# Performance work log

Hardware: AMD Instinct MI355X
Metric: run time of the kernel (lower is better)

## Reference

```python
import jax, jax.numpy as jnp
import numpy as np

jax.config.update("jax_enable_x64", True)

BATCH = 64
NUM_TRAJ = 128
MAXT = 1.0
DELTAT = 2.0 ** -8
N_STEPS = int(round(MAXT / DELTAT)) - 1  # tvec = arange(0, maxt, dt): 256 points -> 255 Euler steps

_sx = np.array([[0, 1], [1, 0]], dtype=np.complex128)
_sy = np.array([[0, -1j], [1j, 0]], dtype=np.complex128)
_sz = np.array([[1, 0], [0, -1]], dtype=np.complex128)
_I2 = np.eye(2, dtype=np.complex128)

# Two-qubit Rabi weak-measurement operators (d=10 Hermitian state, m=2 noise channels)
HX = jnp.asarray(0.5 * (np.kron(_sx, _I2) + np.kron(_I2, _sx)))  # Rabi drive
HZ = jnp.asarray(0.5 * (np.kron(_sz, _I2) + np.kron(_I2, _sz)))  # detuning
C1 = jnp.asarray(np.kron(_sz, _I2))  # weak measurement channel, qubit 0
C2 = jnp.asarray(np.kron(_I2, _sz))  # weak measurement channel, qubit 1


def _meas_ops():
    # 42 probabilities: 9 joint Pauli-basis pairs x 4 outcomes (36) + single-qubit '+' outcomes (6)
    paulis = [_sx, _sy, _sz]
    ops = []
    for A in paulis:
        for B in paulis:
            for sa in (1, -1):
                for sb in (1, -1):
                    ops.append(np.kron((_I2 + sa * A) / 2, (_I2 + sb * B) / 2))
    for A in paulis:
        ops.append(np.kron((_I2 + A) / 2, _I2))
    for B in paulis:
        ops.append(np.kron(_I2, (_I2 + B) / 2))
    return jnp.asarray(np.stack(ops))  # [42, 4, 4]

MEAS = _meas_ops()


def _forward(inputs, params, wvec, rho0):
    inputs = inputs.astype(jnp.float64)  # [B, 1]
    batch = inputs.shape[0]

    # Build per-trajectory params: column input_param=0 comes from inputs, rest are constants
    cols = [inputs + 1e-8 if ii == 0 else params[ii].astype(jnp.float64) * jnp.ones_like(inputs)
            for ii in range(params.shape[0])]
    traj_p = jnp.concatenate(cols, axis=1)            # [B, 4]
    traj_p = jnp.tile(traj_p, (NUM_TRAJ, 1))          # [N, 4], N = NUM_TRAJ*B
    N = NUM_TRAJ * batch

    rho = jnp.tile(rho0[None].astype(jnp.complex128), (N, 1, 1))  # [N, 4, 4]

    Omega = traj_p[:, 0].astype(jnp.complex128)[:, None, None]
    eps = traj_p[:, 1].astype(jnp.complex128)[:, None, None]
    Gamma = traj_p[:, 2][:, None, None]               # real
    eta = traj_p[:, 3][:, None, None]                 # real, measurement efficiency
    H = Omega * HX + eps * HZ                         # [N, 4, 4]
    sqge = jnp.sqrt(jnp.maximum(Gamma * eta, 0.0))

    def hmeas(r, c):
        # H[c] rho = c rho + rho c - tr(c rho + rho c) rho  (c Hermitian)
        anti = c @ r + r @ c
        tr = jnp.trace(anti, axis1=-2, axis2=-1)[:, None, None]
        return anti - tr * r

    def step(r, dw):                                  # dw: [N, 2] real, ~sqrt(dt) Gaussian
        comm = H @ r - r @ H
        diss = (C1 @ r @ C1 - r) + (C2 @ r @ C2 - r)  # c^2 = I for sigma_z channels
        drift = -1j * comm + Gamma * diss
        noise = sqge * (hmeas(r, C1) * dw[:, 0, None, None]
                        + hmeas(r, C2) * dw[:, 1, None, None])
        return r + drift * DELTAT + noise, None

    dws = jnp.swapaxes(wvec.astype(jnp.float64), 0, 1)  # [T-1, N, 2]
    rho_T, _ = jax.lax.scan(step, rho, dws)

    # Monte-Carlo average over num_traj (matches reduce_mean over axis 0 of [num_traj, B, ...])
    rho_mean = jnp.mean(rho_T.reshape(NUM_TRAJ, batch, 4, 4), axis=0)  # [B, 4, 4]

    probs = jnp.real(jnp.einsum('kij,bji->bk', MEAS, rho_mean))        # tr(M rho), [B, 42]
    probs = jnp.clip(probs, 0.0, 1.0)
    out = jnp.concatenate([probs, inputs], axis=1)                     # [B, 43]
    return out, rho_mean


def setup_inputs() -> dict:
    key = jax.random.key(0)
    k1, k2 = jax.random.split(key)
    inputs = jax.random.uniform(k1, (BATCH, 1), dtype=jnp.float64)
    params = jnp.array([1.0, 0.1, 0.5, 0.8], dtype=jnp.float64)  # [Omega, eps, Gamma, eta]
    wvec = jax.random.normal(k2, (NUM_TRAJ * BATCH, N_STEPS, 2), dtype=jnp.float64) * np.sqrt(DELTAT)
    rho0 = jnp.zeros((4, 4), dtype=jnp.complex128).at[0, 0].set(1.0)  # |00><00|
    return {"inputs": inputs, "params": params, "wvec": wvec, "rho0": rho0}


def reference(inputs, params, wvec, rho0):
    return _forward(inputs, params, wvec, rho0)
```

## Files before the change

### kernel.cpp

```cpp
#include <hip/hip_runtime.h>
#include <math.h>

#define BATCH 64
#define NUM_TRAJ 128
#define NTOT (BATCH*NUM_TRAJ)
#define NSTEPS 255

static constexpr float DT = 0.00390625f;

template<int C>
__device__ __forceinline__ float qp(float x) {
    union { float f; int i; } u;
    u.f = x;
    u.i = __builtin_amdgcn_update_dpp(0, u.i, C, 0xF, 0xF, true);
    return u.f;
}
#define DPP_HALF_MIRROR 0x141

__device__ __forceinline__ float qsum2(float x) { return qp<65>(x) + qp<190>(x); }

__global__ __launch_bounds__(64) void traj_kernel(
    const float* __restrict__ inputs,
    const float* __restrict__ params,
    const float* __restrict__ wvec,
    const float* __restrict__ rho0,
    int rho0_cplx,
    float* __restrict__ ws)
{
    const int tid = blockIdx.x * 64 + threadIdx.x;
    const int g  = tid >> 3;
    const int l8 = tid & 7;
    const int p  = l8 & 3;
    const int c  = l8 >> 2;
    const int r  = c ? (3 - p) : p;
    const int b  = g & (BATCH - 1);

    const float Omega = inputs[b] + 1e-8f;
    const float a     = 0.5f * Omega;
    const float eps   = params[1];
    const float Gamma = params[2];
    const float eta   = params[3];
    const float sqge  = sqrtf(fmaxf(Gamma * eta, 0.0f));
    const float gdt   = Gamma * DT;

    const float s1   = (r < 2) ? 1.0f : -1.0f;
    const float s2   = (r & 1) ? -1.0f : 1.0f;
    const float hr   = (r == 0) ? eps : ((r == 3) ? -eps : 0.0f);
    const int  colA  = c ? 1 : 0;
    const int  colB  = c ? 2 : 3;
    const float s2A  = c ? -1.0f : 1.0f;
    const float coefA = hr - (c ? 0.0f : eps);
    const float coefB = hr + (c ? 0.0f : eps);
    const float dmA  = gdt * ( (s1 + s2 * s2A) - 2.0f);
    const float dmB  = gdt * (-(s1 + s2 * s2A) - 2.0f);
    const float S1   = s1 * sqge;
    const float S2   = s2 * sqge;
    const float SQ   = sqge;
    const float PC2  = (c ? -1.0f : 1.0f) * sqge;
    const float f1   = (r == colA) ? 1.0f : 0.0f;
    const float f2   = (r == colB) ? 1.0f : 0.0f;

    float qa_re, qa_im, qb_re, qb_im;
    {
        const int idxA = r * 4 + colA, idxB = r * 4 + colB;
        if (rho0_cplx) {
            qa_re = rho0[2 * idxA]; qa_im = rho0[2 * idxA + 1];
            qb_re = rho0[2 * idxB]; qb_im = rho0[2 * idxB + 1];
        } else {
            qa_re = rho0[idxA]; qa_im = 0.0f;
            qb_re = rho0[idxB]; qb_im = 0.0f;
        }
    }

    const float2* wp2 = reinterpret_cast<const float2*>(wvec) + (size_t)g * NSTEPS;

    auto step = [&](float dwA, float dwB) {
        const float u_re = qa_re + qb_re, u_im = qa_im + qb_im;
        const float up_re = qp<DPP_HALF_MIRROR>(u_re);
        const float up_im = qp<DPP_HALF_MIRROR>(u_im);

        const float pown = fmaf(S1, dwA, S2 * dwB);
        const float tw = pown + pown;
        const float tm_re = tw * fmaf(f1, qa_re, f2 * qb_re);
        const float tm_im = tw * fmaf(f1, qa_im, f2 * qb_im);

        const float SA_re = qsum2(qa_re), SA_im = qsum2(qa_im);
        const float SB_re = qsum2(qb_re), SB_im = qsum2(qb_im);

        const float cA_re = fmaf(coefA, qa_re, a * (SA_re - up_re));
        const float cA_im = fmaf(coefA, qa_im, a * (SA_im - up_im));
        const float cB_re = fmaf(coefB, qb_re, a * (SB_re - up_re));
        const float cB_im = fmaf(coefB, qb_im, a * (SB_im - up_im));

        float z_re = tm_re, z_im = tm_im;
        z_re += qp<177>(z_re); z_im += qp<177>(z_im);
        z_re += qp<78>(z_re);  z_im += qp<78>(z_im);
        z_re += qp<DPP_HALF_MIRROR>(z_re);
        z_im += qp<DPP_HALF_MIRROR>(z_im);
        const float ur = z_re, ui = z_im;

        const float pc   = fmaf(SQ, dwA, PC2 * dwB);
        const float base = pown - ur;
        const float WA = (base + dmA) + pc;
        const float WB = (base + dmB) - pc;

        float n_re, n_im;
        n_re = fmaf(DT, cA_im, qa_re);  n_re = fmaf(WA, qa_re, n_re); n_re = fmaf( ui, qa_im, n_re);
        n_im = fmaf(-DT, cA_re, qa_im); n_im = fmaf(WA, qa_im, n_im); n_im = fmaf(-ui, qa_re, n_im);
        qa_re = n_re; qa_im = n_im;
        n_re = fmaf(DT, cB_im, qb_re);  n_re = fmaf(WB, qb_re, n_re); n_re = fmaf( ui, qb_im, n_re);
        n_im = fmaf(-DT, cB_re, qb_im); n_im = fmaf(WB, qb_im, n_im); n_im = fmaf(-ui, qb_re, n_im);
        qb_re = n_re; qb_im = n_im;
    };

    float2 cw[8], nw[8];
#pragma unroll
    for (int s = 0; s < 8; ++s) cw[s] = wp2[s];
#pragma unroll 1
    for (int T = 0; T < 31; ++T) {
        if (T < 30) {
#pragma unroll
            for (int s = 0; s < 8; ++s) nw[s] = wp2[8 * (T + 1) + s];
        } else {
#pragma unroll
            for (int s = 0; s < 7; ++s) nw[s] = wp2[248 + s];
            nw[7] = make_float2(0.f, 0.f);
        }
#pragma unroll
        for (int s = 0; s < 8; ++s) step(cw[s].x, cw[s].y);
#pragma unroll
        for (int s = 0; s < 8; ++s) cw[s] = nw[s];
    }
#pragma unroll
    for (int s = 0; s < 7; ++s) step(cw[s].x, cw[s].y);

    float4* o = reinterpret_cast<float4*>(ws + (size_t)g * 32);
    o[c * 4 + r] = make_float4(qa_re, qa_im, qb_re, qb_im);
}

__device__ inline void fill_proj(int p, float s, float pr[2][2], float pim[2][2])
{
    pr[0][0] = 0.5f; pr[0][1] = 0.f; pr[1][0] = 0.f; pr[1][1] = 0.5f;
    pim[0][0] = 0.f; pim[0][1] = 0.f; pim[1][0] = 0.f; pim[1][1] = 0.f;
    const float h = 0.5f * s;
    if (p == 0)      { pr[0][1] += h;  pr[1][0] += h; }
    else if (p == 1) { pim[0][1] -= h; pim[1][0] += h; }
    else             { pr[0][0] += h;  pr[1][1] -= h; }
}

__device__ inline void fill_id(float pr[2][2], float pim[2][2])
{
    pr[0][0] = 1.f; pr[0][1] = 0.f; pr[1][0] = 0.f; pr[1][1] = 1.f;
    pim[0][0] = 0.f; pim[0][1] = 0.f; pim[1][0] = 0.f; pim[1][1] = 0.f;
}

__global__ __launch_bounds__(256) void reduce_meas_kernel(
    const float* __restrict__ ws,
    const float* __restrict__ inputs,
    float* __restrict__ out,
    int out_size)
{
    const int b = blockIdx.x;
    const int tid = threadIdx.x;
    __shared__ float part[8][32];
    __shared__ float sr[16], si[16];

    {
        const int e = tid & 31;
        const int h = tid >> 5;
        const int plane = e >> 4;
        const int el = e & 15;
        const int i = el >> 2, j = el & 3;
        const int cc = (j == 1 || j == 2) ? 1 : 0;
        const int slot = (j == 2 || j == 3) ? 1 : 0;
        const int fidx = (cc * 4 + i) * 4 + slot * 2 + plane;
        float s = 0.f;
#pragma unroll 4
        for (int k = h * 16; k < h * 16 + 16; k++)
            s += ws[((size_t)(k * BATCH + b)) * 32 + fidx];
        part[h][e] = s;
    }
    __syncthreads();
    if (tid < 32) {
        float s = 0.f;
#pragma unroll
        for (int h = 0; h < 8; h++) s += part[h][tid];
        s *= (1.0f / NUM_TRAJ);
        if (tid < 16) sr[tid] = s; else si[tid - 16] = s;
    }
    __syncthreads();

    if (tid < 42) {
        float par[2][2], pai[2][2], pbr[2][2], pbi[2][2];
        const int m = tid;
        if (m < 36) {
            const int ia = m / 12, rem = m - ia * 12;
            const int ib = rem / 4, r2 = rem - ib * 4;
            fill_proj(ia, (r2 & 2) ? -1.f : 1.f, par, pai);
            fill_proj(ib, (r2 & 1) ? -1.f : 1.f, pbr, pbi);
        } else if (m < 39) {
            fill_proj(m - 36, 1.f, par, pai);
            fill_id(pbr, pbi);
        } else {
            fill_id(par, pai);
            fill_proj(m - 39, 1.f, pbr, pbi);
        }
        float prob = 0.f;
#pragma unroll
        for (int a1 = 0; a1 < 2; a1++)
#pragma unroll
            for (int b1 = 0; b1 < 2; b1++)
#pragma unroll
                for (int a2 = 0; a2 < 2; a2++)
#pragma unroll
                    for (int b2 = 0; b2 < 2; b2++) {
                        const int i = 2 * a1 + b1, j = 2 * a2 + b2;
                        const float Mr = par[a1][a2] * pbr[b1][b2] - pai[a1][a2] * pbi[b1][b2];
                        const float Mi = par[a1][a2] * pbi[b1][b2] + pai[a1][a2] * pbr[b1][b2];
                        prob += Mr * sr[j * 4 + i] - Mi * si[j * 4 + i];
                    }
        prob = fminf(fmaxf(prob, 0.f), 1.f);
        out[b * 43 + m] = prob;
    } else if (tid == 42) {
        out[b * 43 + 42] = inputs[b];
    }

    if (out_size >= 2752 + 2048) {
        if (tid < 16) {
            out[2752 + b * 32 + 2 * tid]     = sr[tid];
            out[2752 + b * 32 + 2 * tid + 1] = si[tid];
        }
    } else if (out_size >= 2752 + 1024) {
        if (tid < 16) out[2752 + b * 16 + tid] = sr[tid];
    }
}

extern "C" void kernel_launch(void* const* d_in, const int* in_sizes, int n_in,
                              void* d_out, int out_size, void* d_ws, size_t ws_size,
                              hipStream_t stream)
{
    const float* inputs = (const float*)d_in[0];
    const float* params = (const float*)d_in[1];
    const float* wvec   = (const float*)d_in[2];
    const float* rho0   = (const float*)d_in[3];
    const int rho0_cplx = (n_in > 3 && in_sizes[3] >= 32) ? 1 : 0;
    float* ws = (float*)d_ws;

    traj_kernel<<<(NTOT * 8) / 64, 64, 0, stream>>>(inputs, params, wvec, rho0, rho0_cplx, ws);
    reduce_meas_kernel<<<BATCH, 256, 0, stream>>>(ws, inputs, (float*)d_out, out_size);
}
```

Before: 36.01 us.

## Split each trajectory across 16 lanes, one density-matrix element per lane

Each trajectory's 4x4 density matrix is now spread over 16 lanes, one complex element each, where before it was 8 lanes holding two elements each. Cross-lane sums use an added row-rotate-by-8 DPP step, and the workspace layout plus the reduce kernel's indexing are updated to match. The aim is to shorten the serial dependency chain per Euler step and double the number of wavefronts, so latency is hidden better across 255 sequential steps. In exchange, twice as many threads each load the same noise values, and every step needs extra DPP operations.

```diff
diff --git a/kernel.cpp b/kernel.cpp
--- a/kernel.cpp
+++ b/kernel.cpp
@@ -16,6 +16,7 @@
     return u.f;
 }
 #define DPP_HALF_MIRROR 0x141
+#define DPP_ROR8        0x128
 
 __device__ __forceinline__ float qsum2(float x) { return qp<65>(x) + qp<190>(x); }
 
@@ -28,12 +29,15 @@
     float* __restrict__ ws)
 {
     const int tid = blockIdx.x * 64 + threadIdx.x;
-    const int g  = tid >> 3;
-    const int l8 = tid & 7;
-    const int p  = l8 & 3;
-    const int c  = l8 >> 2;
-    const int r  = c ? (3 - p) : p;
-    const int b  = g & (BATCH - 1);
+    const int g   = tid >> 4;
+    const int L   = tid & 15;
+    const int hh  = L >> 3;
+    const int l8  = L & 7;
+    const int p   = l8 & 3;
+    const int c   = l8 >> 2;
+    const int r   = c ? (3 - p) : p;
+    const int col = hh ? (c ? 2 : 3) : (c ? 1 : 0);
+    const int b   = g & (BATCH - 1);
 
     const float Omega = inputs[b] + 1e-8f;
     const float a     = 0.5f * Omega;
@@ -43,74 +47,62 @@
     const float sqge  = sqrtf(fmaxf(Gamma * eta, 0.0f));
     const float gdt   = Gamma * DT;
 
-    const float s1   = (r < 2) ? 1.0f : -1.0f;
-    const float s2   = (r & 1) ? -1.0f : 1.0f;
-    const float hr   = (r == 0) ? eps : ((r == 3) ? -eps : 0.0f);
-    const int  colA  = c ? 1 : 0;
-    const int  colB  = c ? 2 : 3;
-    const float s2A  = c ? -1.0f : 1.0f;
-    const float coefA = hr - (c ? 0.0f : eps);
-    const float coefB = hr + (c ? 0.0f : eps);
-    const float dmA  = gdt * ( (s1 + s2 * s2A) - 2.0f);
-    const float dmB  = gdt * (-(s1 + s2 * s2A) - 2.0f);
-    const float S1   = s1 * sqge;
-    const float S2   = s2 * sqge;
-    const float SQ   = sqge;
-    const float PC2  = (c ? -1.0f : 1.0f) * sqge;
-    const float f1   = (r == colA) ? 1.0f : 0.0f;
-    const float f2   = (r == colB) ? 1.0f : 0.0f;
-
-    float qa_re, qa_im, qb_re, qb_im;
+    const float s1r = (r   < 2) ? 1.0f : -1.0f;
+    const float s2r = (r   & 1) ? -1.0f : 1.0f;
+    const float s1c = (col < 2) ? 1.0f : -1.0f;
+    const float s2c = (col & 1) ? -1.0f : 1.0f;
+    const float hr  = (r   == 0) ? eps : ((r   == 3) ? -eps : 0.0f);
+    const float hc  = (col == 0) ? eps : ((col == 3) ? -eps : 0.0f);
+    const float coef = hr - hc;
+    const float dm  = gdt * (s1r * s1c + s2r * s2c - 2.0f);
+    const float S1  = s1r * sqge;
+    const float S2  = s2r * sqge;
+    const float PA  = s1c * sqge;
+    const float PB  = s2c * sqge;
+    const float f   = (r == col) ? 1.0f : 0.0f;
+    const float FA  = 2.0f * f * S1;
+    const float FB  = 2.0f * f * S2;
+
+    float x_re, x_im;
     {
-        const int idxA = r * 4 + colA, idxB = r * 4 + colB;
-        if (rho0_cplx) {
-            qa_re = rho0[2 * idxA]; qa_im = rho0[2 * idxA + 1];
-            qb_re = rho0[2 * idxB]; qb_im = rho0[2 * idxB + 1];
-        } else {
-            qa_re = rho0[idxA]; qa_im = 0.0f;
-            qb_re = rho0[idxB]; qb_im = 0.0f;
-        }
+        const int idx = r * 4 + col;
+        if (rho0_cplx) { x_re = rho0[2 * idx]; x_im = rho0[2 * idx + 1]; }
+        else           { x_re = rho0[idx];     x_im = 0.0f; }
     }
 
     const float2* wp2 = reinterpret_cast<const float2*>(wvec) + (size_t)g * NSTEPS;
 
     auto step = [&](float dwA, float dwB) {
-        const float u_re = qa_re + qb_re, u_im = qa_im + qb_im;
+        const float u_re = x_re + qp<DPP_ROR8>(x_re);
+        const float u_im = x_im + qp<DPP_ROR8>(x_im);
         const float up_re = qp<DPP_HALF_MIRROR>(u_re);
         const float up_im = qp<DPP_HALF_MIRROR>(u_im);
 
+        const float S_re = qsum2(x_re);
+        const float S_im = qsum2(x_im);
+
+        const float cm_re = fmaf(coef, x_re, a * (S_re - up_re));
+        const float cm_im = fmaf(coef, x_im, a * (S_im - up_im));
+
+        const float t = fmaf(FA, dwA, FB * dwB);
+        float z_re = t * x_re, z_im = t * x_im;
+        z_re += qp<177>(z_re);             z_im += qp<177>(z_im);
+        z_re += qp<78>(z_re);              z_im += qp<78>(z_im);
+        z_re += qp<DPP_HALF_MIRROR>(z_re); z_im += qp<DPP_HALF_MIRROR>(z_im);
+        z_re += qp<DPP_ROR8>(z_re);        z_im += qp<DPP_ROR8>(z_im);
+        const float ur = z_re, ui = z_im;
+
         const float pown = fmaf(S1, dwA, S2 * dwB);
-        const float tw = pown + pown;
-        const float tm_re = tw * fmaf(f1, qa_re, f2 * qb_re);
-        const float tm_im = tw * fmaf(f1, qa_im, f2 * qb_im);
-
-        const float SA_re = qsum2(qa_re), SA_im = qsum2(qa_im);
-        const float SB_re = qsum2(qb_re), SB_im = qsum2(qb_im);
-
-        const float cA_re = fmaf(coefA, qa_re, a * (SA_re - up_re));
-        const float cA_im = fmaf(coefA, qa_im, a * (SA_im - up_im));
-        const float cB_re = fmaf(coefB, qb_re, a * (SB_re - up_re));
-        const float cB_im = fmaf(coefB, qb_im, a * (SB_im - up_im));
-
-        float z_re = tm_re, z_im = tm_im;
-        z_re += qp<177>(z_re); z_im += qp<177>(z_im);
-        z_re += qp<78>(z_re);  z_im += qp<78>(z_im);
-        z_re += qp<DPP_HALF_MIRROR>(z_re);
-        z_im += qp<DPP_HALF_MIRROR>(z_im);
-        const float ur = z_re, ui = z_im;
-
-        const float pc   = fmaf(SQ, dwA, PC2 * dwB);
-        const float base = pown - ur;
-        const float WA = (base + dmA) + pc;
-        const float WB = (base + dmB) - pc;
-
-        float n_re, n_im;
-        n_re = fmaf(DT, cA_im, qa_re);  n_re = fmaf(WA, qa_re, n_re); n_re = fmaf( ui, qa_im, n_re);
-        n_im = fmaf(-DT, cA_re, qa_im); n_im = fmaf(WA, qa_im, n_im); n_im = fmaf(-ui, qa_re, n_im);
-        qa_re = n_re; qa_im = n_im;
-        n_re = fmaf(DT, cB_im, qb_re);  n_re = fmaf(WB, qb_re, n_re); n_re = fmaf( ui, qb_im, n_re);
-        n_im = fmaf(-DT, cB_re, qb_im); n_im = fmaf(WB, qb_im, n_im); n_im = fmaf(-ui, qb_re, n_im);
-        qb_re = n_re; qb_im = n_im;
+        const float pcol = fmaf(PA, dwA, PB * dwB);
+        const float W = (pown - ur) + (pcol + dm);
+
+        float n_re = fmaf(DT, cm_im, x_re);
+        n_re = fmaf(W, x_re, n_re);
+        n_re = fmaf(ui, x_im, n_re);
+        float n_im = fmaf(-DT, cm_re, x_im);
+        n_im = fmaf(W, x_im, n_im);
+        n_im = fmaf(-ui, x_re, n_im);
+        x_re = n_re; x_im = n_im;
     };
 
     float2 cw[8], nw[8];
@@ -134,8 +126,7 @@
 #pragma unroll
     for (int s = 0; s < 7; ++s) step(cw[s].x, cw[s].y);
 
-    float4* o = reinterpret_cast<float4*>(ws + (size_t)g * 32);
-    o[c * 4 + r] = make_float4(qa_re, qa_im, qb_re, qb_im);
+    reinterpret_cast<float2*>(ws + (size_t)g * 32)[L] = make_float2(x_re, x_im);
 }
 
 __device__ inline void fill_proj(int p, float s, float pr[2][2], float pim[2][2])
@@ -172,8 +163,9 @@
         const int el = e & 15;
         const int i = el >> 2, j = el & 3;
         const int cc = (j == 1 || j == 2) ? 1 : 0;
-        const int slot = (j == 2 || j == 3) ? 1 : 0;
-        const int fidx = (cc * 4 + i) * 4 + slot * 2 + plane;
+        const int hh = (j == 2 || j == 3) ? 1 : 0;
+        const int p  = cc ? (3 - i) : i;
+        const int fidx = (hh * 8 + cc * 4 + p) * 2 + plane;
         float s = 0.f;
 #pragma unroll 4
         for (int k = h * 16; k < h * 16 + 16; k++)
@@ -246,6 +238,6 @@
     const int rho0_cplx = (n_in > 3 && in_sizes[3] >= 32) ? 1 : 0;
     float* ws = (float*)d_ws;
 
-    traj_kernel<<<(NTOT * 8) / 64, 64, 0, stream>>>(inputs, params, wvec, rho0, rho0_cplx, ws);
+    traj_kernel<<<(NTOT * 16) / 64, 64, 0, stream>>>(inputs, params, wvec, rho0, rho0_cplx, ws);
     reduce_meas_kernel<<<BATCH, 256, 0, stream>>>(ws, inputs, (float*)d_out, out_size);
 }
```

Result: slower. 46.83 us (+30.1%).
